# Kernel optimization log

Measured on AMD Instinct MI355X. Metric: run time of the kernel, lower is better.

The kernel has to match this reference:

```python
import jax, jax.numpy as jnp
import numpy as np

N = 16384      # total ligand atoms
E = 65536      # edges
B = 256        # graphs / batch
MAXN = 64      # atoms per graph (max_nodes for to_dense_batch)
FIN = 64       # num_node_features
HID = 256      # hidden_channels
GH = 2         # gat heads
LP = 1024      # protein length
NH = 4         # cross-attention heads
HD = HID // NH
VOCAB = 22


def setup_inputs() -> dict:
    key = jax.random.key(0)
    ks = jax.random.split(key, 48)
    f = jnp.float32
    def nrm(k, shape, s=0.05):
        return jax.random.normal(k, shape, f) * s
    inp = {}
    inp["x"] = jax.random.normal(ks[0], (N, FIN), f)
    inp["edge_index"] = jax.random.randint(ks[1], (2, E), 0, N)
    inp["batch"] = jnp.arange(N) // MAXN  # sorted, 64 atoms per graph
    inp["protein_seq"] = jax.random.randint(ks[2], (B, LP), 0, VOCAB)
    # GAT layer 1 (FIN -> HID, GH heads, concat=False)
    inp["w1"] = nrm(ks[3], (FIN, GH * HID)); inp["as1"] = nrm(ks[4], (GH, HID)); inp["ad1"] = nrm(ks[5], (GH, HID)); inp["b1"] = jnp.zeros((HID,), f)
    inp["w2"] = nrm(ks[6], (HID, GH * HID)); inp["as2"] = nrm(ks[7], (GH, HID)); inp["ad2"] = nrm(ks[8], (GH, HID)); inp["b2"] = jnp.zeros((HID,), f)
    inp["w3"] = nrm(ks[9], (HID, GH * HID)); inp["as3"] = nrm(ks[10], (GH, HID)); inp["ad3"] = nrm(ks[11], (GH, HID)); inp["b3"] = jnp.zeros((HID,), f)
    # protein embedding + conv1d (OIH layout)
    inp["emb"] = nrm(ks[12], (VOCAB, HID), 0.1)
    inp["conv_w"] = nrm(ks[13], (HID, HID, 3)); inp["conv_b"] = jnp.zeros((HID,), f)
    # cross-attention MHA
    inp["wq"] = nrm(ks[14], (HID, HID)); inp["bq"] = jnp.zeros((HID,), f)
    inp["wk"] = nrm(ks[15], (HID, HID)); inp["bk"] = jnp.zeros((HID,), f)
    inp["wv"] = nrm(ks[16], (HID, HID)); inp["bv"] = jnp.zeros((HID,), f)
    inp["wo"] = nrm(ks[17], (HID, HID)); inp["bo"] = jnp.zeros((HID,), f)
    inp["ln1_g"] = jnp.ones((HID,), f); inp["ln1_b"] = jnp.zeros((HID,), f)
    inp["ffw1"] = nrm(ks[18], (HID, 4 * HID)); inp["ffb1"] = jnp.zeros((4 * HID,), f)
    inp["ffw2"] = nrm(ks[19], (4 * HID, HID)); inp["ffb2"] = jnp.zeros((HID,), f)
    inp["ln2_g"] = jnp.ones((HID,), f); inp["ln2_b"] = jnp.zeros((HID,), f)
    inp["fc1_w"] = nrm(ks[20], (HID, HID)); inp["fc1_b"] = jnp.zeros((HID,), f)
    inp["fc2_w"] = nrm(ks[21], (HID, 1)); inp["fc2_b"] = jnp.zeros((1,), f)
    return inp


def _gat(x, edge_index, W, a_src, a_dst, bias):
    # PyG GATConv, concat=False (mean over heads), add_self_loops=True
    n = x.shape[0]
    h = (x @ W).reshape(n, GH, HID)                      # [N,GH,C]
    loop = jnp.arange(n)
    src = jnp.concatenate([edge_index[0], loop])
    dst = jnp.concatenate([edge_index[1], loop])
    a_s = jnp.einsum('nhc,hc->nh', h, a_src)             # [N,GH]
    a_d = jnp.einsum('nhc,hc->nh', h, a_dst)
    e = jax.nn.leaky_relu(a_s[src] + a_d[dst], 0.2)      # [E+N,GH]
    emax = jax.ops.segment_max(e, dst, num_segments=n)   # each node has a self-loop
    ex = jnp.exp(e - emax[dst])
    den = jax.ops.segment_sum(ex, dst, num_segments=n)
    alpha = ex / den[dst]                                # [E+N,GH]
    msg = h[src] * alpha[:, :, None]
    out = jax.ops.segment_sum(msg, dst, num_segments=n)  # [N,GH,C]
    return out.mean(axis=1) + bias


def _to_dense_batch(x, batch):
    # batch is sorted node->graph ids; counts per graph <= MAXN
    ones = jnp.ones((x.shape[0],), jnp.int32)
    counts = jax.ops.segment_sum(ones, batch, num_segments=B)
    starts = jnp.cumsum(counts) - counts
    pos = jnp.arange(x.shape[0]) - starts[batch]
    dense = jnp.zeros((B, MAXN, x.shape[1]), x.dtype).at[batch, pos].set(x)
    mask = jnp.zeros((B, MAXN), bool).at[batch, pos].set(True)
    return dense, mask


def _layernorm(x, g, b, eps=1e-5):
    mu = x.mean(-1, keepdims=True)
    var = ((x - mu) ** 2).mean(-1, keepdims=True)
    return (x - mu) * jax.lax.rsqrt(var + eps) * g + b


def reference(x, edge_index, batch, protein_seq,
              w1, as1, ad1, b1, w2, as2, ad2, b2, w3, as3, ad3, b3,
              emb, conv_w, conv_b,
              wq, bq, wk, bk, wv, bv, wo, bo,
              ln1_g, ln1_b, ffw1, ffb1, ffw2, ffb2, ln2_g, ln2_b,
              fc1_w, fc1_b, fc2_w, fc2_b):
    # --- ligand GNN (eval mode: dropout = identity) ---
    h = jax.nn.elu(_gat(x, edge_index, w1, as1, ad1, b1))
    h = jax.nn.elu(_gat(h, edge_index, w2, as2, ad2, b2))
    h = jax.nn.elu(_gat(h, edge_index, w3, as3, ad3, b3))
    lig, lig_mask = _to_dense_batch(h, batch)            # [B,MAXN,HID], [B,MAXN]
    # --- protein branch ---
    p = emb[protein_seq]                                 # [B,LP,HID]
    p = p.transpose(0, 2, 1)                             # [B,HID,LP]
    p = jax.lax.conv_general_dilated(p, conv_w, (1,), [(1, 1)],
                                     dimension_numbers=('NCH', 'OIH', 'NCH'))
    p = jax.nn.relu(p + conv_b[None, :, None]).transpose(0, 2, 1)  # [B,LP,HID]
    kpm = protein_seq == 0                               # key padding mask
    # --- cross attention (query=ligand, key/value=protein) ---
    q = (lig @ wq + bq).reshape(B, MAXN, NH, HD)
    k = (p @ wk + bk).reshape(B, LP, NH, HD)
    v = (p @ wv + bv).reshape(B, LP, NH, HD)
    scores = jnp.einsum('bqhd,bkhd->bhqk', q, k) / np.sqrt(HD).astype(np.float32)
    scores = jnp.where(kpm[:, None, None, :], jnp.float32(-1e9), scores)
    attn = jax.nn.softmax(scores, axis=-1)               # [B,NH,MAXN,LP]
    ctx = jnp.einsum('bhqk,bkhd->bqhd', attn, v).reshape(B, MAXN, HID)
    attn_out = ctx @ wo + bo
    y = _layernorm(lig + attn_out, ln1_g, ln1_b)
    ff = jax.nn.gelu(y @ ffw1 + ffb1, approximate=False) @ ffw2 + ffb2
    y = _layernorm(y + ff, ln2_g, ln2_b)
    # --- masked mean pool ---
    m = lig_mask[:, :, None].astype(y.dtype)
    pooled = (y * m).sum(axis=1) / (m.sum(axis=1) + 1e-6)
    out = jax.nn.relu(pooled @ fc1_w + fc1_b)
    return out @ fc2_w + fc2_b                           # [B,1]
```

## Files before the change

kernel.cpp:

```cpp
#include <hip/hip_runtime.h>
#include <hip/hip_bf16.h>
#include <cstdint>
#include <cstddef>

#define NAT 16384
#define NED 65536
#define BGR 256
#define FIN 64
#define HID 256
#define LPN 1024
#define HD 64
#define NTRIP 11638
#define NTAB  11648

typedef __bf16 bf16x8 __attribute__((ext_vector_type(8)));
typedef float floatx4 __attribute__((ext_vector_type(4)));

__device__ __forceinline__ void gl2lds16(const void* g, void* l)
{
    __builtin_amdgcn_global_load_lds(
        (const __attribute__((address_space(1))) unsigned int*)g,
        (__attribute__((address_space(3))) unsigned int*)l, 16, 0, 0);
}

template<int ACT, int OUTBF16, int BIASROW, int HSPLIT>
__global__ __launch_bounds__(512) void gemm_mfma(const __bf16* __restrict__ A,
    const __bf16* __restrict__ Bt, const float* __restrict__ bias,
    void* __restrict__ Cout, int M, int Nn, int K, float escale)
{
    __shared__ __bf16 As[2][128][32];
    __shared__ __bf16 Bs[2][128][32];
    const int t = threadIdx.x;
    const int m0 = blockIdx.y * 128, n0 = blockIdx.x * 128;
    const int w = t >> 6, lane = t & 63;
    const int wm = (w & 3) * 32, wn = (w >> 2) * 64;
    const int quad = lane >> 4, l16 = lane & 15;
    const int r0 = t >> 2, s0 = t & 3, g0 = (s0 ^ (r0 & 3)) * 8;
    const int fso = (quad ^ (l16 & 3)) * 8;
    floatx4 acc[2][4] = {};
    for (int k0 = 0; k0 < K; k0 += 64) {
        gl2lds16(A + (size_t)(m0 + r0) * K + k0 + g0,       &As[0][r0][s0 * 8]);
        gl2lds16(A + (size_t)(m0 + r0) * K + k0 + 32 + g0,  &As[1][r0][s0 * 8]);
        gl2lds16(Bt + (size_t)(n0 + r0) * K + k0 + g0,      &Bs[0][r0][s0 * 8]);
        gl2lds16(Bt + (size_t)(n0 + r0) * K + k0 + 32 + g0, &Bs[1][r0][s0 * 8]);
        __syncthreads();
#pragma unroll
        for (int c = 0; c < 2; c++) {
            bf16x8 af[2], bfr[4];
#pragma unroll
            for (int mi = 0; mi < 2; mi++) af[mi]  = *(const bf16x8*)&As[c][wm + mi * 16 + l16][fso];
#pragma unroll
            for (int nj = 0; nj < 4; nj++) bfr[nj] = *(const bf16x8*)&Bs[c][wn + nj * 16 + l16][fso];
#pragma unroll
            for (int mi = 0; mi < 2; mi++)
#pragma unroll
                for (int nj = 0; nj < 4; nj++)
                    acc[mi][nj] = __builtin_amdgcn_mfma_f32_16x16x32_bf16(af[mi], bfr[nj], acc[mi][nj], 0, 0, 0);
        }
        __syncthreads();
    }
#pragma unroll
    for (int mi = 0; mi < 2; mi++)
#pragma unroll
        for (int nj = 0; nj < 4; nj++) {
            int col = n0 + wn + nj * 16 + l16;
#pragma unroll
            for (int r = 0; r < 4; r++) {
                int row = m0 + wm + mi * 16 + quad * 4 + r;
                float bval = bias ? (BIASROW ? bias[row] : bias[col]) : 0.f;
                float v = (acc[mi][nj][r] + bval) * escale;
                if (ACT == 1) v = fmaxf(v, 0.f);
                if (ACT == 2) v = 0.5f * v * (1.f + erff(v * 0.70710678118654752f));
                if (HSPLIT)      ((__bf16*)Cout)[((size_t)(col >> 6) * M + row) * 64 + (col & 63)] = (__bf16)v;
                else if (OUTBF16) ((__bf16*)Cout)[(size_t)row * Nn + col] = (__bf16)v;
                else              ((float*)Cout)[(size_t)row * Nn + col] = v;
            }
        }
}

__global__ __launch_bounds__(512) void gemm_gat(const __bf16* __restrict__ A,
    const __bf16* __restrict__ Bt, const float* __restrict__ as_f,
    const float* __restrict__ ad_f, __bf16* __restrict__ Hg,
    float* __restrict__ part, int K)
{
    __shared__ __bf16 As[2][128][32];
    __shared__ __bf16 Bs[2][128][32];
    const int t = threadIdx.x;
    const int m0 = blockIdx.y * 128, n0 = blockIdx.x * 128;
    const int w = t >> 6, lane = t & 63;
    const int wm = (w & 3) * 32, wn = (w >> 2) * 64;
    const int quad = lane >> 4, l16 = lane & 15;
    const int r0 = t >> 2, s0 = t & 3, g0 = (s0 ^ (r0 & 3)) * 8;
    const int fso = (quad ^ (l16 & 3)) * 8;
    floatx4 acc[2][4] = {};
    for (int k0 = 0; k0 < K; k0 += 64) {
        gl2lds16(A + (size_t)(m0 + r0) * K + k0 + g0,       &As[0][r0][s0 * 8]);
        gl2lds16(A + (size_t)(m0 + r0) * K + k0 + 32 + g0,  &As[1][r0][s0 * 8]);
        gl2lds16(Bt + (size_t)(n0 + r0) * K + k0 + g0,      &Bs[0][r0][s0 * 8]);
        gl2lds16(Bt + (size_t)(n0 + r0) * K + k0 + 32 + g0, &Bs[1][r0][s0 * 8]);
        __syncthreads();
#pragma unroll
        for (int c = 0; c < 2; c++) {
            bf16x8 af[2], bfr[4];
#pragma unroll
            for (int mi = 0; mi < 2; mi++) af[mi]  = *(const bf16x8*)&As[c][wm + mi * 16 + l16][fso];
#pragma unroll
            for (int nj = 0; nj < 4; nj++) bfr[nj] = *(const bf16x8*)&Bs[c][wn + nj * 16 + l16][fso];
#pragma unroll
            for (int mi = 0; mi < 2; mi++)
#pragma unroll
                for (int nj = 0; nj < 4; nj++)
                    acc[mi][nj] = __builtin_amdgcn_mfma_f32_16x16x32_bf16(af[mi], bfr[nj], acc[mi][nj], 0, 0, 0);
        }
        __syncthreads();
    }
    const int slot = blockIdx.x * 2 + (w >> 2);
#pragma unroll
    for (int mi = 0; mi < 2; mi++) {
#pragma unroll
        for (int r = 0; r < 4; r++) {
            float ps = 0.f, pd = 0.f;
#pragma unroll
            for (int nj = 0; nj < 4; nj++) {
                int col = n0 + wn + nj * 16 + l16;
                float v = acc[mi][nj][r];
                ps += v * as_f[col];
                pd += v * ad_f[col];
            }
#pragma unroll
            for (int off = 1; off < 16; off <<= 1) {
                ps += __shfl_xor(ps, off, 64);
                pd += __shfl_xor(pd, off, 64);
            }
            if (l16 == 0) {
                int row = m0 + wm + mi * 16 + quad * 4 + r;
                part[(size_t)(slot * 2 + 0) * NAT + row] = ps;
                part[(size_t)(slot * 2 + 1) * NAT + row] = pd;
            }
        }
    }
#pragma unroll
    for (int mi = 0; mi < 2; mi++)
#pragma unroll
        for (int nj = 0; nj < 4; nj++) {
            int col = n0 + wn + nj * 16 + l16;
#pragma unroll
            for (int r = 0; r < 4; r++) {
                int row = m0 + wm + mi * 16 + quad * 4 + r;
                Hg[(size_t)row * 512 + col] = (__bf16)acc[mi][nj][r];
            }
        }
}

__global__ void fold_k(const float* __restrict__ part, float* __restrict__ a_s,
                       float* __restrict__ a_d)
{
    int n = blockIdx.x * 256 + threadIdx.x;
    float s0 = 0.f, d0 = 0.f, s1 = 0.f, d1 = 0.f;
#pragma unroll
    for (int sl = 0; sl < 4; sl++) {
        s0 += part[(size_t)(sl * 2 + 0) * NAT + n];
        d0 += part[(size_t)(sl * 2 + 1) * NAT + n];
        s1 += part[(size_t)((sl + 4) * 2 + 0) * NAT + n];
        d1 += part[(size_t)((sl + 4) * 2 + 1) * NAT + n];
    }
    a_s[n * 2 + 0] = s0; a_s[n * 2 + 1] = s1;
    a_d[n * 2 + 0] = d0; a_d[n * 2 + 1] = d1;
}

__global__ __launch_bounds__(256) void tap_k(const float* __restrict__ emb,
    const float* __restrict__ cw, float* __restrict__ tap)
{
    const int dlv = blockIdx.x >> 2, part = blockIdx.x & 3;
    const int dl = dlv / 22, v = dlv % 22;
    const int n = threadIdx.x;
    const float* er = emb + v * 256 + part * 64;
    const float* wr = cw + (size_t)n * 768 + part * 192 + dl;
    float s = 0.f;
    for (int k = 0; k < 64; k += 4) {
        s += er[k + 0] * wr[k * 3 + 0];
        s += er[k + 1] * wr[k * 3 + 3];
        s += er[k + 2] * wr[k * 3 + 6];
        s += er[k + 3] * wr[k * 3 + 9];
    }
    atomicAdd(&tap[(size_t)dlv * 256 + n], s);
}

__global__ __launch_bounds__(256) void ptab_k(const float* __restrict__ tap,
    const float* __restrict__ bias, __bf16* __restrict__ P)
{
    const int t = threadIdx.x;
    const int row = blockIdx.x * 8 + (t >> 5);
    const int c = (t & 31) * 8;
    __bf16 o[8];
    if (row < NTRIP) {
        const int a = row / 506, rem = row - a * 506;
        const int t1 = rem / 23, c2 = rem - t1 * 23;
        float acc[8];
#pragma unroll
        for (int j = 0; j < 8; j++) acc[j] = bias[c + j];
        if (a > 0) {
            const float* r = tap + (size_t)(0 * 22 + (a - 1)) * 256 + c;
#pragma unroll
            for (int j = 0; j < 8; j++) acc[j] += r[j];
        }
        {
            const float* r = tap + (size_t)(1 * 22 + t1) * 256 + c;
#pragma unroll
            for (int j = 0; j < 8; j++) acc[j] += r[j];
        }
        if (c2 > 0) {
            const float* r = tap + (size_t)(2 * 22 + (c2 - 1)) * 256 + c;
#pragma unroll
            for (int j = 0; j < 8; j++) acc[j] += r[j];
        }
#pragma unroll
        for (int j = 0; j < 8; j++) o[j] = (__bf16)fmaxf(acc[j], 0.f);
    } else {
#pragma unroll
        for (int j = 0; j < 8; j++) o[j] = (__bf16)0.f;
    }
    *(uint4*)(P + (size_t)row * 256 + c) = *(uint4*)o;
}

__global__ void tid_k(const int* __restrict__ seq, unsigned short* __restrict__ tid)
{
    int i = blockIdx.x * 256 + threadIdx.x;
    int b = i >> 10, l = i & 1023;
    const int* sr = seq + b * LPN;
    int t0 = (l > 0) ? sr[l - 1] : -1;
    int t1 = sr[l];
    int t2 = (l < LPN - 1) ? sr[l + 1] : -1;
    int v = (t0 + 1) * 506 + t1 * 23 + (t2 + 1);
    tid[i] = (unsigned short)(v | (t1 == 0 ? 0x8000 : 0));
}

struct Segs {
    const float* src[12];
    __bf16* dst[12];
    int kdim[12];
    int ndim[12];
    int mode[12];
    int start[13];
};

__global__ void cvtall_k(Segs S, int total)
{
    int i = blockIdx.x * 256 + threadIdx.x;
    if (i >= total) return;
    int s = 0;
    while (i >= S.start[s + 1]) s++;
    int j = i - S.start[s];
    if (S.mode[s] == 0) {
        S.dst[s][j] = (__bf16)S.src[s][j];
    } else {
        int K = S.kdim[s], N = S.ndim[s];
        int n = j / K, k = j - n * K;
        S.dst[s][j] = (__bf16)S.src[s][(size_t)k * N + n];
    }
}

__global__ void deg_k(const int* __restrict__ ei, int* __restrict__ deg)
{
    int e = blockIdx.x * 256 + threadIdx.x;
    if (e < NED) atomicAdd(&deg[ei[NED + e]], 1);
}

__global__ __launch_bounds__(256) void scan_k(const int* __restrict__ deg, int* __restrict__ rowptr)
{
    __shared__ int part[256];
    int t = threadIdx.x;
    int base = t * 64;
    int s = 0;
#pragma unroll
    for (int i = 0; i < 64; i++) s += deg[base + i];
    part[t] = s;
    __syncthreads();
    for (int off = 1; off < 256; off <<= 1) {
        int v = (t >= off) ? part[t - off] : 0;
        __syncthreads();
        part[t] += v;
        __syncthreads();
    }
    int run = t ? part[t - 1] : 0;
    for (int i = 0; i < 64; i++) { rowptr[base + i] = run; run += deg[base + i]; }
    if (t == 255) rowptr[16384] = run;
}

__global__ void scat_k(const int* __restrict__ ei, int* __restrict__ fill,
                       const int* __restrict__ rowptr, int* __restrict__ csrc,
                       int* __restrict__ cdst)
{
    int e = blockIdx.x * 256 + threadIdx.x;
    if (e >= NED) return;
    int d = ei[NED + e];
    int pos = rowptr[d] + atomicAdd(&fill[d], 1);
    csrc[pos] = ei[e];
    cdst[pos] = d;
}

__global__ void erec_k(const int* __restrict__ csrc, const int* __restrict__ cdst,
    const float* __restrict__ a_s, const float* __restrict__ a_d,
    float4* __restrict__ rec)
{
    int p = blockIdx.x * 256 + threadIdx.x;
    if (p >= NED) return;
    int s = csrc[p], d = cdst[p];
    float2 as2 = *(const float2*)(a_s + s * 2);
    float2 ad2 = *(const float2*)(a_d + d * 2);
    float e0 = as2.x + ad2.x; e0 = (e0 > 0.f) ? e0 : 0.2f * e0;
    float e1 = as2.y + ad2.y; e1 = (e1 > 0.f) ? e1 : 0.2f * e1;
    rec[p] = make_float4(e0, e1, __int_as_float(s), 0.f);
}

__global__ __launch_bounds__(256) void gat_agg(const int* __restrict__ rowptr,
    const float4* __restrict__ rec, const __bf16* __restrict__ hgb,
    const float* __restrict__ a_s, const float* __restrict__ a_d,
    const float* __restrict__ bias, float* __restrict__ out, __bf16* __restrict__ outb)
{
    const int wave = threadIdx.x >> 6, lane = threadIdx.x & 63;
    const int d = blockIdx.x * 4 + wave;
    const int beg = rowptr[d], end = rowptr[d + 1];
    float2 as2 = *(const float2*)(a_s + d * 2);
    float2 ad2 = *(const float2*)(a_d + d * 2);
    float e0 = as2.x + ad2.x; e0 = (e0 > 0.f) ? e0 : 0.2f * e0;
    float e1 = as2.y + ad2.y; e1 = (e1 > 0.f) ? e1 : 0.2f * e1;
    float m0 = e0, den0 = 1.f, m1 = e1, den1 = 1.f;
    for (int p = beg; p < end; p++) {
        float4 rc = rec[p];
        float nm0 = fmaxf(m0, rc.x);
        den0 = den0 * __expf(m0 - nm0) + __expf(rc.x - nm0);
        m0 = nm0;
        float nm1 = fmaxf(m1, rc.y);
        den1 = den1 * __expf(m1 - nm1) + __expf(rc.y - nm1);
        m1 = nm1;
    }
    const float inv0 = 1.f / den0, inv1 = 1.f / den1;
    const int ch = lane * 8;
    const int g = ch >> 8;
    const float mg = g ? m1 : m0, invg = g ? inv1 : inv0;
    float acc[8] = {};
    {
        float al = __expf((g ? e1 : e0) - mg) * invg;
        bf16x8 hv = *(const bf16x8*)(hgb + (size_t)d * 512 + ch);
#pragma unroll
        for (int j = 0; j < 8; j++) acc[j] += (float)hv[j] * al;
    }
    for (int p = beg; p < end; p++) {
        float4 rc = rec[p];
        float al = __expf((g ? rc.y : rc.x) - mg) * invg;
        int s = __float_as_int(rc.z);
        bf16x8 hv = *(const bf16x8*)(hgb + (size_t)s * 512 + ch);
#pragma unroll
        for (int j = 0; j < 8; j++) acc[j] += (float)hv[j] * al;
    }
    float other[8];
#pragma unroll
    for (int j = 0; j < 8; j++) other[j] = __shfl_xor(acc[j], 32, 64);
    if (lane < 32) {
#pragma unroll
        for (int j = 0; j < 8; j++) {
            float v = 0.5f * (acc[j] + other[j]) + bias[ch + j];
            v = (v > 0.f) ? v : expm1f(v);
            if (out) out[(size_t)d * 256 + ch + j] = v;
            outb[(size_t)d * 256 + ch + j] = (__bf16)v;
        }
    }
}

__global__ __launch_bounds__(256, 4) void attn6_k(const __bf16* __restrict__ Qb,
    const __bf16* __restrict__ Ktab, const __bf16* __restrict__ Vtab,
    const unsigned short* __restrict__ tid16, __bf16* __restrict__ O)
{
    __shared__ __bf16 Ks[2][4096];
    __shared__ __bf16 Vs[4096];
    __shared__ __bf16 Ps2[4][16][64];
    __shared__ float mask_f[1024];
    __shared__ unsigned short tids[1024];
    const int t = threadIdx.x;
    const int bid = blockIdx.x;
    const int h = (bid >> 1) & 3;
    const int b = ((bid >> 3) << 1) | (bid & 1);
    const int w = t >> 6, lane = t & 63;
    const int quad = lane >> 4, l16 = lane & 15;
    const int key = (l16 & 7) << 4;
    const __bf16* Kh = Ktab + (size_t)h * NTAB * 64;
    const __bf16* Vh = Vtab + (size_t)h * NTAB * 64;
    {
        const uint32_t* src = (const uint32_t*)(tid16 + (size_t)b * LPN);
        uint32_t v0 = src[t], v1 = src[t + 256];
        ((uint32_t*)tids)[t] = v0;
        ((uint32_t*)tids)[t + 256] = v1;
        mask_f[2 * t + 0] = (v0 & 0x8000u) ? -1e9f : 0.f;
        mask_f[2 * t + 1] = (v0 & 0x80000000u) ? -1e9f : 0.f;
        mask_f[2 * (t + 256) + 0] = (v1 & 0x8000u) ? -1e9f : 0.f;
        mask_f[2 * (t + 256) + 1] = (v1 & 0x80000000u) ? -1e9f : 0.f;
    }
    const __bf16* qrow = Qb + (size_t)(b * 64 + w * 16 + l16) * HID + h * HD;
    bf16x8 aq0 = *(const bf16x8*)(qrow + quad * 8);
    bf16x8 aq1 = *(const bf16x8*)(qrow + 32 + quad * 8);
    __syncthreads();

    auto stageK = [&](int kt, int bufb) {
#pragma unroll
        for (int it = 0; it < 2; it++) {
            const int s = it * 256 + t;
            const int pos = s >> 3;
            const int c = (s & 7) ^ (pos & 7);
            const int row = tids[kt * 64 + pos] & 0x7fff;
            gl2lds16(Kh + (size_t)row * 64 + c * 8,
                     &Ks[bufb][(it * 256 + w * 64) * 8]);
        }
    };
    auto loadV = [&](int kt, bf16x8* vrr) {
#pragma unroll
        for (int it = 0; it < 2; it++) {
            const int pos = w * 8 + (lane >> 3) + it * 32;
            const int row = tids[kt * 64 + pos] & 0x7fff;
            vrr[it] = *(const bf16x8*)(Vh + (size_t)row * 64 + (lane & 7) * 8);
        }
    };
    auto writeV = [&](const bf16x8* vrr) {
        const int p = lane >> 3, c = lane & 7;
#pragma unroll
        for (int it = 0; it < 2; it++) {
            const int pos = w * 8 + p + it * 32;
            const int cp = pos >> 3;
#pragma unroll
            for (int j = 0; j < 8; j++) {
                const int chl = c * 8 + j;
                Vs[chl * 64 + (((cp ^ c ^ j) & 7) << 3) + p] = vrr[it][j];
            }
        }
    };

    bf16x8 vr[2];
    stageK(0, 0);
    loadV(0, vr);
    writeV(vr);
    float m_run = -3e38f;
    float l_run = 0.f;
    floatx4 ctx[4] = {};
    __syncthreads();

    for (int kt = 0; kt < 16; kt++) {
        const int buf = kt & 1;
        const int kp0 = kt * 64;
        if (kt < 15) {
            stageK(kt + 1, buf ^ 1);
            loadV(kt + 1, vr);
        }
        const int ksl0 = (quad ^ (l16 & 7)) * 8;
        const int ksl1 = ((quad + 4) ^ (l16 & 7)) * 8;
        floatx4 s[4];
#pragma unroll
        for (int nj = 0; nj < 4; nj++) {
            const __bf16* kr = &Ks[buf][(nj * 16 + l16) * 64];
            bf16x8 k0 = *(const bf16x8*)&kr[ksl0];
            bf16x8 k1 = *(const bf16x8*)&kr[ksl1];
            floatx4 z = {0.f, 0.f, 0.f, 0.f};
            s[nj] = __builtin_amdgcn_mfma_f32_16x16x32_bf16(k0, aq0, z, 0, 0, 0);
            s[nj] = __builtin_amdgcn_mfma_f32_16x16x32_bf16(k1, aq1, s[nj], 0, 0, 0);
        }
#pragma unroll
        for (int nj = 0; nj < 4; nj++) {
            floatx4 m4 = *(const floatx4*)&mask_f[kp0 + nj * 16 + quad * 4];
#pragma unroll
            for (int r = 0; r < 4; r++) s[nj][r] += m4[r];
        }
        float mx = -3e38f;
#pragma unroll
        for (int nj = 0; nj < 4; nj++)
#pragma unroll
            for (int r = 0; r < 4; r++) mx = fmaxf(mx, s[nj][r]);
        mx = fmaxf(mx, __shfl_xor(mx, 16, 64));
        mx = fmaxf(mx, __shfl_xor(mx, 32, 64));
        const float mn = fmaxf(m_run, mx);
        const float alpha = __expf(m_run - mn);
        m_run = mn;
        float rs = 0.f;
#pragma unroll
        for (int nj = 0; nj < 4; nj++)
#pragma unroll
            for (int r = 0; r < 4; r++) {
                float p = __expf(s[nj][r] - mn);
                s[nj][r] = p;
                rs += p;
            }
        rs += __shfl_xor(rs, 16, 64);
        rs += __shfl_xor(rs, 32, 64);
        l_run = l_run * alpha + rs;
        float al[4];
#pragma unroll
        for (int r = 0; r < 4; r++) al[r] = __shfl(alpha, quad * 4 + r, 64);
        {
            char* rowp = (char*)&Ps2[w][l16][0];
#pragma unroll
            for (int nj = 0; nj < 4; nj++) {
                union { uint2 u2; unsigned short us[4]; } pk;
#pragma unroll
                for (int r = 0; r < 4; r++) {
                    __bf16 bv = (__bf16)s[nj][r];
                    pk.us[r] = *(unsigned short*)&bv;
                }
                *(uint2*)(rowp + ((nj * 32 + quad * 8) ^ key)) = pk.u2;
            }
        }
        bf16x8 pa0 = *(const bf16x8*)((char*)&Ps2[w][l16][0] + ((quad * 16) ^ key));
        bf16x8 pa1 = *(const bf16x8*)((char*)&Ps2[w][l16][0] + ((64 + quad * 16) ^ key));
#pragma unroll
        for (int dj = 0; dj < 4; dj++) {
#pragma unroll
            for (int r = 0; r < 4; r++) ctx[dj][r] *= al[r];
            const int chl = dj * 16 + l16;
            const int Xc = ((chl >> 3) ^ (chl & 7)) & 7;
            bf16x8 bv0 = *(const bf16x8*)&Vs[chl * 64 + (((quad ^ Xc) & 7) << 3)];
            bf16x8 bv1 = *(const bf16x8*)&Vs[chl * 64 + ((((quad + 4) ^ Xc) & 7) << 3)];
            ctx[dj] = __builtin_amdgcn_mfma_f32_16x16x32_bf16(pa0, bv0, ctx[dj], 0, 0, 0);
            ctx[dj] = __builtin_amdgcn_mfma_f32_16x16x32_bf16(pa1, bv1, ctx[dj], 0, 0, 0);
        }
        __syncthreads();
        if (kt < 15) writeV(vr);
        __syncthreads();
    }
    float ll[4];
#pragma unroll
    for (int r = 0; r < 4; r++) ll[r] = __shfl(l_run, quad * 4 + r, 64);
#pragma unroll
    for (int dj = 0; dj < 4; dj++)
#pragma unroll
        for (int r = 0; r < 4; r++) {
            int q = w * 16 + quad * 4 + r;
            O[((size_t)(b * 64 + q)) * 256 + h * HD + dj * 16 + l16] = (__bf16)(ctx[dj][r] / ll[r]);
        }
}

__device__ __forceinline__ float blockSum256(float v, float* red)
{
#pragma unroll
    for (int off = 32; off >= 1; off >>= 1) v += __shfl_down(v, off, 64);
    int wave = threadIdx.x >> 6, lane = threadIdx.x & 63;
    if (lane == 0) red[wave] = v;
    __syncthreads();
    float s = red[0] + red[1] + red[2] + red[3];
    __syncthreads();
    return s;
}

__global__ __launch_bounds__(256) void lnres_k(const float* __restrict__ A,
    const float* __restrict__ Bb, const float* __restrict__ g,
    const float* __restrict__ be, float* __restrict__ Y, __bf16* __restrict__ Yb)
{
    __shared__ float red[4];
    int r = blockIdx.x, t = threadIdx.x;
    float v = A[(size_t)r * 256 + t] + Bb[(size_t)r * 256 + t];
    float mean = blockSum256(v, red) * (1.f / 256.f);
    float d = v - mean;
    float var = blockSum256(d * d, red) * (1.f / 256.f);
    float o = d * rsqrtf(var + 1e-5f) * g[t] + be[t];
    Y[(size_t)r * 256 + t] = o;
    if (Yb) Yb[(size_t)r * 256 + t] = (__bf16)o;
}

__global__ __launch_bounds__(256) void head_k(const float* __restrict__ Y,
    const float* __restrict__ fc1w, const float* __restrict__ fc1b,
    const float* __restrict__ fc2w, const float* __restrict__ fc2b,
    float* __restrict__ out)
{
    __shared__ float pooled[256];
    __shared__ float h[256];
    __shared__ float red[4];
    int b = blockIdx.x, t = threadIdx.x;
    float s = 0.f;
#pragma unroll 8
    for (int q = 0; q < 64; q++) s += Y[(size_t)(b * 64 + q) * 256 + t];
    pooled[t] = s / (64.f + 1e-6f);
    __syncthreads();
    float a = 0.f;
    for (int k = 0; k < 256; k += 4) {
        a += pooled[k + 0] * fc1w[(k + 0) * 256 + t];
        a += pooled[k + 1] * fc1w[(k + 1) * 256 + t];
        a += pooled[k + 2] * fc1w[(k + 2) * 256 + t];
        a += pooled[k + 3] * fc1w[(k + 3) * 256 + t];
    }
    h[t] = fmaxf(a + fc1b[t], 0.f);
    __syncthreads();
    float p = h[t] * fc2w[t];
    p = blockSum256(p, red);
    if (t == 0) out[b] = p + fc2b[0];
}

extern "C" void kernel_launch(void* const* d_in, const int* in_sizes, int n_in,
                              void* d_out, int out_size, void* d_ws, size_t ws_size,
                              hipStream_t stream)
{
    const float* x     = (const float*)d_in[0];
    const int*   ei    = (const int*)d_in[1];
    const int*   pseq  = (const int*)d_in[3];
    const float* w1  = (const float*)d_in[4];
    const float* as1 = (const float*)d_in[5];
    const float* ad1 = (const float*)d_in[6];
    const float* b1  = (const float*)d_in[7];
    const float* w2  = (const float*)d_in[8];
    const float* as2 = (const float*)d_in[9];
    const float* ad2 = (const float*)d_in[10];
    const float* b2  = (const float*)d_in[11];
    const float* w3  = (const float*)d_in[12];
    const float* as3 = (const float*)d_in[13];
    const float* ad3 = (const float*)d_in[14];
    const float* b3  = (const float*)d_in[15];
    const float* emb    = (const float*)d_in[16];
    const float* conv_w = (const float*)d_in[17];
    const float* conv_b = (const float*)d_in[18];
    const float* wq = (const float*)d_in[19];
    const float* bq = (const float*)d_in[20];
    const float* wk = (const float*)d_in[21];
    const float* bk = (const float*)d_in[22];
    const float* wv = (const float*)d_in[23];
    const float* bv = (const float*)d_in[24];
    const float* wo = (const float*)d_in[25];
    const float* bo = (const float*)d_in[26];
    const float* ln1_g = (const float*)d_in[27];
    const float* ln1_b = (const float*)d_in[28];
    const float* ffw1  = (const float*)d_in[29];
    const float* ffb1  = (const float*)d_in[30];
    const float* ffw2  = (const float*)d_in[31];
    const float* ffb2  = (const float*)d_in[32];
    const float* ln2_g = (const float*)d_in[33];
    const float* ln2_b = (const float*)d_in[34];
    const float* fc1_w = (const float*)d_in[35];
    const float* fc1_b = (const float*)d_in[36];
    const float* fc2_w = (const float*)d_in[37];
    const float* fc2_b = (const float*)d_in[38];
    (void)in_sizes; (void)n_in; (void)out_size;

    char* ws = (char*)d_ws;
    size_t off = 0;
    auto alloc = [&](size_t bytes) -> char* {
        char* p = ws + off;
        off += (bytes + 255) & ~(size_t)255;
        return p;
    };
    __bf16* hgb  = (__bf16*)alloc((size_t)NAT * 512 * 2);
    float* og    = (float*)alloc((size_t)NAT * 512 * 4);
    float* hb0   = (float*)alloc((size_t)NAT * 256 * 4);
    float* hb1   = (float*)alloc((size_t)NAT * 256 * 4);
    __bf16* xb   = (__bf16*)alloc((size_t)NAT * FIN * 2);
    __bf16* hbb  = (__bf16*)alloc((size_t)NAT * 256 * 2);
    __bf16* qbb  = (__bf16*)alloc((size_t)NAT * 256 * 2);
    __bf16* ctxbb= (__bf16*)alloc((size_t)NAT * 256 * 2);
    __bf16* ybb  = (__bf16*)alloc((size_t)NAT * 256 * 2);
    float* a_s   = (float*)alloc((size_t)NAT * 2 * 4);
    float* a_d   = (float*)alloc((size_t)NAT * 2 * 4);
    float* asd_p = (float*)alloc((size_t)16 * NAT * 4);
    int* deg     = (int*)alloc((size_t)NAT * 4);
    int* fill    = (int*)alloc((size_t)NAT * 4);
    int* rowptr  = (int*)alloc((size_t)(NAT + 1) * 4);
    int* csrc    = (int*)alloc((size_t)NED * 4);
    int* cdst    = (int*)alloc((size_t)NED * 4);
    float4* erec = (float4*)alloc((size_t)NED * 16);
    float* tap   = (float*)alloc((size_t)3 * 22 * 256 * 4);
    __bf16* ptab = (__bf16*)alloc((size_t)NTAB * 256 * 2);
    __bf16* Ktab = (__bf16*)alloc((size_t)NTAB * 256 * 2);
    __bf16* Vtab = (__bf16*)alloc((size_t)NTAB * 256 * 2);
    unsigned short* tid16 = (unsigned short*)alloc((size_t)BGR * LPN * 2);
    __bf16* w1T  = (__bf16*)alloc((size_t)512 * 64 * 2);
    __bf16* w2T  = (__bf16*)alloc((size_t)512 * 256 * 2);
    __bf16* w3T  = (__bf16*)alloc((size_t)512 * 256 * 2);
    __bf16* wkT  = (__bf16*)alloc((size_t)256 * 256 * 2);
    __bf16* wvT  = (__bf16*)alloc((size_t)256 * 256 * 2);
    __bf16* wqT  = (__bf16*)alloc((size_t)256 * 256 * 2);
    __bf16* woT  = (__bf16*)alloc((size_t)256 * 256 * 2);
    __bf16* f1T  = (__bf16*)alloc((size_t)1024 * 256 * 2);
    __bf16* f2T  = (__bf16*)alloc((size_t)256 * 1024 * 2);
    size_t fixed_end = off;
    char* region   = ws + fixed_end;
    __bf16* ffbb   = (__bf16*)region;
    float*  y2     = (float*)(region + (size_t)NAT * 1024 * 2);
    float* attno = og;
    float* ybuf  = og + (size_t)NAT * 256;
    float* ff2o  = hb1;
    (void)ws_size;

    hipMemsetAsync(deg, 0, (size_t)NAT * 8, stream);
    hipMemsetAsync(tap, 0, (size_t)3 * 22 * 256 * 4, stream);
    deg_k<<<NED / 256, 256, 0, stream>>>(ei, deg);
    scan_k<<<1, 256, 0, stream>>>(deg, rowptr);
    scat_k<<<NED / 256, 256, 0, stream>>>(ei, fill, rowptr, csrc, cdst);
    tap_k<<<264, 256, 0, stream>>>(emb, conv_w, tap);

    {
        Segs S;
        const float* srcs[10] = {x, w1, w2, w3, wk, wv, wq, wo, ffw1, ffw2};
        __bf16* dsts[10] = {xb, w1T, w2T, w3T, wkT, wvT, wqT, woT, f1T, f2T};
        int kd[10] = {0, 64, 256, 256, 256, 256, 256, 256, 256, 1024};
        int nd[10] = {0, 512, 512, 512, 256, 256, 256, 256, 1024, 256};
        int md[10] = {0, 1, 1, 1, 1, 1, 1, 1, 1, 1};
        int cnt[10] = {NAT * FIN, 32768, 131072, 131072,
                       65536, 65536, 65536, 65536, 262144, 262144};
        int run = 0;
        for (int i = 0; i < 10; i++) {
            S.src[i] = srcs[i]; S.dst[i] = dsts[i];
            S.kdim[i] = kd[i]; S.ndim[i] = nd[i]; S.mode[i] = md[i];
            S.start[i] = run; run += cnt[i];
        }
        S.start[10] = run; S.start[11] = run; S.start[12] = run;
        cvtall_k<<<(run + 255) / 256, 256, 0, stream>>>(S, run);
    }

    ptab_k<<<NTAB / 8, 256, 0, stream>>>(tap, conv_b, ptab);
    tid_k<<<BGR * LPN / 256, 256, 0, stream>>>(pseq, tid16);
    gemm_mfma<0, 1, 0, 1><<<dim3(2, NTAB / 128), 512, 0, stream>>>(ptab, wkT, bk, Ktab, NTAB, 256, 256, 1.f);
    gemm_mfma<0, 1, 0, 1><<<dim3(2, NTAB / 128), 512, 0, stream>>>(ptab, wvT, bv, Vtab, NTAB, 256, 256, 1.f);

    const __bf16* WT[3] = {w1T, w2T, w3T};
    const float* asl[3] = {as1, as2, as3};
    const float* adl[3] = {ad1, ad2, ad3};
    const float* bl[3]  = {b1, b2, b3};
    float* houts[3] = {nullptr, nullptr, hb0};
    const __bf16* hinb = xb;
    int Kdim = FIN;
    for (int l = 0; l < 3; l++) {
        gemm_gat<<<dim3(4, NAT / 128), 512, 0, stream>>>(hinb, WT[l], asl[l], adl[l], hgb, asd_p, Kdim);
        fold_k<<<NAT / 256, 256, 0, stream>>>(asd_p, a_s, a_d);
        erec_k<<<NED / 256, 256, 0, stream>>>(csrc, cdst, a_s, a_d, erec);
        gat_agg<<<NAT / 4, 256, 0, stream>>>(rowptr, erec, hgb, a_s, a_d, bl[l], houts[l], hbb);
        hinb = hbb;
        Kdim = HID;
    }
    const float* lig = hb0;
    const __bf16* ligb = hbb;

    gemm_mfma<0, 1, 0, 0><<<dim3(2, NAT / 128), 512, 0, stream>>>(ligb, wqT, bq, qbb, NAT, 256, 256, 0.125f);

    attn6_k<<<BGR * 4, 256, 0, stream>>>(qbb, Ktab, Vtab, tid16, ctxbb);

    gemm_mfma<0, 0, 0, 0><<<dim3(2, NAT / 128), 512, 0, stream>>>(ctxbb, woT, bo, attno, NAT, 256, 256, 1.f);
    lnres_k<<<NAT, 256, 0, stream>>>(lig, attno, ln1_g, ln1_b, ybuf, ybb);
    gemm_mfma<2, 1, 0, 0><<<dim3(8, NAT / 128), 512, 0, stream>>>(ybb, f1T, ffb1, ffbb, NAT, 1024, 256, 1.f);
    gemm_mfma<0, 0, 0, 0><<<dim3(2, NAT / 128), 512, 0, stream>>>(ffbb, f2T, ffb2, ff2o, NAT, 256, 1024, 1.f);
    lnres_k<<<NAT, 256, 0, stream>>>(ybuf, ff2o, ln2_g, ln2_b, y2, nullptr);

    head_k<<<BGR, 256, 0, stream>>>(y2, fc1_w, fc1_b, fc2_w, fc2_b, (float*)d_out);
}
```

Before: 505.4 us.

## Fuse FFN up-projection, GELU and down-projection into one kernel

```diff
diff --git a/kernel.cpp b/kernel.cpp
--- a/kernel.cpp
+++ b/kernel.cpp
@@ -74,6 +74,101 @@
                 if (HSPLIT)      ((__bf16*)Cout)[((size_t)(col >> 6) * M + row) * 64 + (col & 63)] = (__bf16)v;
                 else if (OUTBF16) ((__bf16*)Cout)[(size_t)row * Nn + col] = (__bf16)v;
                 else              ((float*)Cout)[(size_t)row * Nn + col] = v;
+            }
+        }
+}
+
+__global__ __launch_bounds__(512) void ffn_k(const __bf16* __restrict__ A,
+    const __bf16* __restrict__ W1t, const __bf16* __restrict__ W2t,
+    const float* __restrict__ b1, const float* __restrict__ b2,
+    float* __restrict__ Cout)
+{
+    __shared__ __bf16 As[64 * 256];
+    __shared__ __bf16 Hs[64 * 128];
+    const int t = threadIdx.x;
+    const int m0 = blockIdx.x * 64;
+    const int w = t >> 6, lane = t & 63;
+    const int rg = w & 1, cg = w >> 1;
+    const int quad = lane >> 4, l16 = lane & 15;
+#pragma unroll
+    for (int it = 0; it < 4; it++) {
+        const int idx = it * 512 + t;
+        const int row = idx >> 5, cs = idx & 31;
+        const int c = (cs & 24) | ((cs & 7) ^ (row & 7));
+        gl2lds16(A + (size_t)(m0 + row) * 256 + c * 8, &As[idx * 8]);
+    }
+    floatx4 acc2[2][4] = {};
+    __syncthreads();
+    const int arow0 = rg * 32 + l16;
+    for (int ch = 0; ch < 8; ch++) {
+        floatx4 acc1[2][2] = {};
+#pragma unroll
+        for (int w32 = 0; w32 < 8; w32++) {
+            bf16x8 a[2];
+#pragma unroll
+            for (int mi = 0; mi < 2; mi++) {
+                const int row = arow0 + mi * 16;
+                const int c = w32 * 4 + quad;
+                const int slot = (c & 24) | ((c & 7) ^ (row & 7));
+                a[mi] = *(const bf16x8*)&As[row * 256 + slot * 8];
+            }
+#pragma unroll
+            for (int nj = 0; nj < 2; nj++) {
+                const int hcol = ch * 128 + cg * 32 + nj * 16 + l16;
+                bf16x8 bfrag = *(const bf16x8*)(W1t + (size_t)hcol * 256 + w32 * 32 + quad * 8);
+#pragma unroll
+                for (int mi = 0; mi < 2; mi++)
+                    acc1[mi][nj] = __builtin_amdgcn_mfma_f32_16x16x32_bf16(a[mi], bfrag, acc1[mi][nj], 0, 0, 0);
+            }
+        }
+#pragma unroll
+        for (int nj = 0; nj < 2; nj++) {
+            const int col = cg * 32 + nj * 16 + l16;
+            const float bv = b1[ch * 128 + col];
+            const int ch8 = col >> 3;
+#pragma unroll
+            for (int mi = 0; mi < 2; mi++)
+#pragma unroll
+                for (int r = 0; r < 4; r++) {
+                    const int row = rg * 32 + mi * 16 + quad * 4 + r;
+                    float v = acc1[mi][nj][r] + bv;
+                    v = 0.5f * v * (1.f + erff(v * 0.70710678118654752f));
+                    const int slot = (ch8 & 8) | ((ch8 & 7) ^ (row & 7));
+                    Hs[row * 128 + slot * 8 + (col & 7)] = (__bf16)v;
+                }
+        }
+        __syncthreads();
+#pragma unroll
+        for (int ks = 0; ks < 4; ks++) {
+            bf16x8 a[2];
+#pragma unroll
+            for (int mi = 0; mi < 2; mi++) {
+                const int row = arow0 + mi * 16;
+                const int c8 = ks * 4 + quad;
+                const int slot = (c8 & 8) | ((c8 & 7) ^ (row & 7));
+                a[mi] = *(const bf16x8*)&Hs[row * 128 + slot * 8];
+            }
+#pragma unroll
+            for (int nj = 0; nj < 4; nj++) {
+                const int ocol = cg * 64 + nj * 16 + l16;
+                bf16x8 bfrag = *(const bf16x8*)(W2t + (size_t)ocol * 1024 + ch * 128 + ks * 32 + quad * 8);
+#pragma unroll
+                for (int mi = 0; mi < 2; mi++)
+                    acc2[mi][nj] = __builtin_amdgcn_mfma_f32_16x16x32_bf16(a[mi], bfrag, acc2[mi][nj], 0, 0, 0);
+            }
+        }
+        __syncthreads();
+    }
+#pragma unroll
+    for (int mi = 0; mi < 2; mi++)
+#pragma unroll
+        for (int nj = 0; nj < 4; nj++) {
+            const int col = cg * 64 + nj * 16 + l16;
+            const float bv = b2[col];
+#pragma unroll
+            for (int r = 0; r < 4; r++) {
+                const int row = m0 + rg * 32 + mi * 16 + quad * 4 + r;
+                Cout[(size_t)row * 256 + col] = acc2[mi][nj][r] + bv;
             }
         }
 }
@@ -675,7 +770,6 @@
     __bf16* f2T  = (__bf16*)alloc((size_t)256 * 1024 * 2);
     size_t fixed_end = off;
     char* region   = ws + fixed_end;
-    __bf16* ffbb   = (__bf16*)region;
     float*  y2     = (float*)(region + (size_t)NAT * 1024 * 2);
     float* attno = og;
     float* ybuf  = og + (size_t)NAT * 256;
@@ -737,8 +831,7 @@
 
     gemm_mfma<0, 0, 0, 0><<<dim3(2, NAT / 128), 512, 0, stream>>>(ctxbb, woT, bo, attno, NAT, 256, 256, 1.f);
     lnres_k<<<NAT, 256, 0, stream>>>(lig, attno, ln1_g, ln1_b, ybuf, ybb);
-    gemm_mfma<2, 1, 0, 0><<<dim3(8, NAT / 128), 512, 0, stream>>>(ybb, f1T, ffb1, ffbb, NAT, 1024, 256, 1.f);
-    gemm_mfma<0, 0, 0, 0><<<dim3(2, NAT / 128), 512, 0, stream>>>(ffbb, f2T, ffb2, ff2o, NAT, 256, 1024, 1.f);
+    ffn_k<<<NAT / 64, 512, 0, stream>>>(ybb, f1T, f2T, ffb1, ffb2, ff2o);
     lnres_k<<<NAT, 256, 0, stream>>>(ybuf, ff2o, ln2_g, ln2_b, y2, nullptr);
 
     head_k<<<BGR, 256, 0, stream>>>(y2, fc1_w, fc1_b, fc2_w, fc2_b, (float*)d_out);
```

Result: slower. 537.3 us (+6.3%).
